# Kernel tuning notes

Hardware: AMD Instinct MI355X
Metric: run time of the kernel (lower is better)

The kernel has to match this reference:

```python
import jax, jax.numpy as jnp
import numpy as np

B, C, H, W = 4, 256, 64, 64
NHEAD = 8
KH = KW = 3          # partition = [3, 3] -> 9-token windows, stride 1, padding 1
EPS = 1e-5           # torch LayerNorm default


def setup_inputs() -> dict:
    key = jax.random.key(0)
    ks = jax.random.split(key, 3)
    s = 1.0 / np.sqrt(C)  # xavier-ish scale
    return {
        "src": jax.random.normal(ks[0], (B, C, H, W), jnp.float32),
        "ln_w": jnp.ones((C,), jnp.float32),
        "ln_b": jnp.zeros((C,), jnp.float32),
        "in_proj_w": jax.random.normal(ks[1], (3 * C, C), jnp.float32) * s,
        "in_proj_b": jnp.zeros((3 * C,), jnp.float32),
        "out_proj_w": jax.random.normal(ks[2], (C, C), jnp.float32) * s,
        "out_proj_b": jnp.zeros((C,), jnp.float32),
    }


def reference(src, ln_w, ln_b, in_proj_w, in_proj_b, out_proj_w, out_proj_b):
    b, c, h, w = src.shape
    L = h * w
    S = KH * KW  # 9 tokens per local window
    # --- Unfold: overlapping 3x3 windows, padding 1, stride 1 (torch.nn.Unfold order: c major, kernel pos minor)
    xp = jnp.pad(src, ((0, 0), (0, 0), (1, 1), (1, 1)))
    patches = jnp.stack(
        [xp[:, :, i : i + h, j : j + w] for i in range(KH) for j in range(KW)], axis=2
    )  # [b, c, 9, h, w]
    x = patches.reshape(b, c, S, L).transpose(2, 0, 3, 1).reshape(S, b * L, c)  # [S, bL, c]
    # --- Pre-norm (norm1); note: pos embed in the source is overwritten (q = k = src2), FFN is dead code
    mu = x.mean(-1, keepdims=True)
    var = ((x - mu) ** 2).mean(-1, keepdims=True)
    x2 = (x - mu) / jnp.sqrt(var + EPS) * ln_w + ln_b
    # --- MultiheadAttention (self-attn, eval mode -> no dropout)
    qkv = jnp.einsum("sbc,dc->sbd", x2, in_proj_w) + in_proj_b  # [S, bL, 3c]
    q, k, v = jnp.split(qkv, 3, axis=-1)
    dh = c // NHEAD
    scale = dh ** -0.5
    q = q.reshape(S, b * L, NHEAD, dh) * scale
    k = k.reshape(S, b * L, NHEAD, dh)
    v = v.reshape(S, b * L, NHEAD, dh)
    scores = jnp.einsum("sbhd,tbhd->bhst", q, k)        # [bL, H, 9, 9]
    attn = jax.nn.softmax(scores, axis=-1)
    o = jnp.einsum("bhst,tbhd->sbhd", attn, v).reshape(S, b * L, c)
    o = jnp.einsum("sbc,dc->sbd", o, out_proj_w) + out_proj_b
    y = x + o  # residual
    # --- Fold back (kernel 1x1, stride 1): each output pixel = its window's center token
    center = y[S // 2]  # [bL, c]
    return center.reshape(b, L, c).transpose(0, 2, 1).reshape(b, c, h, w)
```

## Files before the change

### kernel.cpp

```cpp
#include <hip/hip_runtime.h>
#include <math.h>


#define NPIX 16384
#define HW   4096
#define CDIM 256

typedef short  bf16x8 __attribute__((ext_vector_type(8)));
typedef float  f32x4  __attribute__((ext_vector_type(4)));
typedef unsigned short u16x8 __attribute__((ext_vector_type(8)));

__device__ inline float bf2f(unsigned short u) {
    unsigned v = ((unsigned)u) << 16;
    return __builtin_bit_cast(float, v);
}
__device__ inline unsigned short f2bf(float f) {
    unsigned u = __builtin_bit_cast(unsigned, f);
    u += 0x7FFFu + ((u >> 16) & 1u);
    return (unsigned short)(u >> 16);
}

__device__ inline void wave_fence_vm0() {
    asm volatile("s_waitcnt vmcnt(0)" ::: "memory");
    __builtin_amdgcn_sched_barrier(0);
}

__global__ __launch_bounds__(256) void k_prep(const float* __restrict__ Wqkv,
                                              const float* __restrict__ Wout,
                                              const float* __restrict__ bqkv,
                                              const float* __restrict__ lnb,
                                              unsigned short* __restrict__ Wqkvbf,
                                              unsigned short* __restrict__ Woutbf,
                                              float* __restrict__ pads) {
    int bid = blockIdx.x, t = threadIdx.x;
    if (bid < 768) {
        int i = bid * 256 + t;
        Wqkvbf[i] = f2bf(Wqkv[i]);
    } else if (bid < 1024) {
        int i = (bid - 768) * 256 + t;
        Woutbf[i] = f2bf(Wout[i]);
    } else {
        int tg = (bid - 1024) * 256 + t;
        int d = tg >> 4, part = tg & 15;
        int row = 256 + d;
        const float* wr = Wqkv + (size_t)row * CDIM + part * 16;
        float s = 0.f;
        #pragma unroll
        for (int c = 0; c < 16; ++c) s += lnb[part * 16 + c] * wr[c];
        s += __shfl_xor(s, 1);
        s += __shfl_xor(s, 2);
        s += __shfl_xor(s, 4);
        s += __shfl_xor(s, 8);
        if (part == 0) pads[d] = s + bqkv[row];
    }
}

__device__ inline void stage32(const unsigned short* __restrict__ g, int grow0,
                               int koff, unsigned short* dst, int lane) {
    int r16  = lane >> 2;
    int slot = lane & 3;
    #pragma unroll
    for (int it = 0; it < 4; ++it) {
        int row = it * 16 + r16;
        const unsigned short* src = g + (size_t)(grow0 + row) * 256 + koff
                                      + ((slot ^ ((row >> 1) & 3)) * 8);
        __builtin_amdgcn_global_load_lds(
            (const __attribute__((address_space(1))) void*)src,
            (__attribute__((address_space(3))) void*)(dst + it * 16 * 32),
            16, 0, 0);
    }
}

__global__ __launch_bounds__(256, 3) void k_ln_qkv(const float* __restrict__ src,
                                                   const float* __restrict__ lnw,
                                                   const float* __restrict__ lnb,
                                                   const unsigned short* __restrict__ Wbf,
                                                   const float* __restrict__ bias,
                                                   unsigned short* __restrict__ qkvbf) {
    __shared__ unsigned short As[32 * 256];
    __shared__ unsigned short Bs[4 * 4096];
    __shared__ float redS[8 * 33 * 2 + 64];

    int t = threadIdx.x;
    int bid = blockIdx.x;
    int sb = (bid & 7) * 64 + (bid >> 3);
    int n0 = sb * 32;
    int b = n0 >> 12, p0 = n0 & 4095;
    int lane = t & 63, wv = t >> 6;
    int lr = lane & 15, lg = lane >> 4;
    unsigned short* BsW = Bs + wv * 4096;

    stage32(Wbf, wv * 64, 0, BsW, lane);

    {
        float* red  = redS;
        float* red2 = redS + 264;
        float* muv  = redS + 528;
        float* rsv  = redS + 560;
        int pix = t & 31, q = t >> 5;
        const float* sp = src + ((size_t)b * CDIM) * HW + p0 + pix;
        float x[32];
        float sum = 0.f, sq = 0.f;
        #pragma unroll
        for (int i = 0; i < 32; ++i) {
            x[i] = sp[(size_t)(q * 32 + i) * HW];
            sum += x[i]; sq += x[i] * x[i];
        }
        red[q * 33 + pix] = sum; red2[q * 33 + pix] = sq;
        __syncthreads();
        if (t < 32) {
            float s = 0.f, s2 = 0.f;
            #pragma unroll
            for (int qq = 0; qq < 8; ++qq) { s += red[qq * 33 + t]; s2 += red2[qq * 33 + t]; }
            float mu = s * (1.f / 256.f);
            float var = fmaxf(s2 * (1.f / 256.f) - mu * mu, 0.f);
            muv[t] = mu; rsv[t] = rsqrtf(var + 1e-5f);
        }
        __syncthreads();
        float mu = muv[pix], rs = rsv[pix];
        #pragma unroll
        for (int c8 = 0; c8 < 4; ++c8) {
            u16x8 o8;
            #pragma unroll
            for (int j = 0; j < 8; ++j) {
                int c = q * 32 + c8 * 8 + j;
                float xn = (x[c8 * 8 + j] - mu) * rs * lnw[c] + lnb[c];
                o8[j] = f2bf(xn);
            }
            int chunk = q * 4 + c8;
            *(u16x8*)((char*)As + (pix * 512 + (((chunk & 7) ^ (pix & 7)) | (chunk & 24)) * 16)) = o8;
        }
    }
    __syncthreads();

    for (int pass = 0; pass < 3; ++pass) {
        int d0 = pass * 256;
        f32x4 acc[2][4] = {};
        #pragma unroll
        for (int kc = 0; kc < 8; ++kc) {
            int g = pass * 8 + kc;
            wave_fence_vm0();
            const unsigned short* B = BsW + (g & 1) * 2048;
            int chA = kc * 4 + lg;
            bf16x8 a[2], bb[4];
            #pragma unroll
            for (int i = 0; i < 2; ++i) {
                int r = i * 16 + lr;
                int sl = ((chA & 7) ^ (r & 7)) | (chA & 24);
                a[i] = *(bf16x8*)((char*)As + (r * 512 + sl * 16));
            }
            #pragma unroll
            for (int j = 0; j < 4; ++j) {
                int rb = j * 16 + lr;
                int sl = lg ^ ((rb >> 1) & 3);
                bb[j] = *(bf16x8*)(B + rb * 32 + sl * 8);
            }
            if (kc < 7)
                stage32(Wbf, d0 + wv * 64, (kc + 1) * 32,
                        BsW + ((g + 1) & 1) * 2048, lane);
            #pragma unroll
            for (int i = 0; i < 2; ++i)
                #pragma unroll
                for (int j = 0; j < 4; ++j)
                    acc[i][j] = __builtin_amdgcn_mfma_f32_16x16x32_bf16(
                        a[i], bb[j], acc[i][j], 0, 0, 0);
        }
        unsigned short* Ct = BsW;
        #pragma unroll
        for (int j = 0; j < 4; ++j) {
            float bj = bias[d0 + wv * 64 + j * 16 + lr];
            #pragma unroll
            for (int i = 0; i < 2; ++i)
                #pragma unroll
                for (int r2 = 0; r2 < 4; ++r2)
                    Ct[(i * 16 + lg * 4 + r2) * 72 + j * 16 + lr] =
                        f2bf(acc[i][j][r2] + bj);
        }
        #pragma unroll
        for (int it2 = 0; it2 < 4; ++it2) {
            int row = 8 * it2 + (lane >> 3);
            int chunk = lane & 7;
            bf16x8 v = *(bf16x8*)(Ct + row * 72 + chunk * 8);
            *(bf16x8*)(qkvbf + (size_t)(n0 + row) * 768 + d0 + wv * 64 + chunk * 8) = v;
        }
        if (pass < 2)
            stage32(Wbf, (pass + 1) * 256 + wv * 64, 0, BsW, lane);
    }
}

__global__ __launch_bounds__(256, 3) void k_attn_proj(const unsigned short* __restrict__ qkvbf,
                                                      const float* __restrict__ pads,
                                                      const unsigned short* __restrict__ Wbf,
                                                      const float* __restrict__ bias,
                                                      const float* __restrict__ src,
                                                      float* __restrict__ out) {
    __shared__ unsigned short Bt[32 * 264];
    __shared__ unsigned short Ws[4 * 4096];
    int t  = threadIdx.x;
    int bid = blockIdx.x;
    int sb  = (bid & 7) * 64 + (bid >> 3);
    int n0 = sb * 32;
    int b  = n0 >> 12;
    int p0 = n0 & 4095;
    int lane = t & 63, wv = t >> 6;
    int lr = lane & 15, lg = lane >> 4;
    unsigned short* WsW = Ws + wv * 4096;

    stage32(Wbf, wv * 64, 0, WsW, lane);

    {
        int pix = t >> 3, h = t & 7;
        int n = n0 + pix;
        int p = n & 4095, hh0 = p >> 6, ww0 = p & 63;
        const float scale = 0.1767766952966369f;

        float qv[32];
        const unsigned short* qp = qkvbf + (size_t)n * 768 + h * 32;
        #pragma unroll
        for (int c8 = 0; c8 < 4; ++c8) {
            bf16x8 v = *(const bf16x8*)(qp + c8 * 8);
            #pragma unroll
            for (int j = 0; j < 8; ++j) qv[c8 * 8 + j] = bf2f((unsigned short)v[j]) * scale;
        }
        float sc[9];
        #pragma unroll
        for (int t9 = 0; t9 < 9; ++t9) {
            int dy = t9 / 3 - 1, dx = t9 % 3 - 1;
            int hh = hh0 + dy, ww = ww0 + dx;
            bool ok = ((unsigned)hh < 64u) && ((unsigned)ww < 64u);
            float a = 0.f;
            if (ok) {
                const unsigned short* kp = qkvbf + (size_t)(n + dy * 64 + dx) * 768 + 256 + h * 32;
                #pragma unroll
                for (int c8 = 0; c8 < 4; ++c8) {
                    bf16x8 v = *(const bf16x8*)(kp + c8 * 8);
                    #pragma unroll
                    for (int j = 0; j < 8; ++j) a += qv[c8 * 8 + j] * bf2f((unsigned short)v[j]);
                }
            } else {
                const float* pk = pads + h * 32;
                #pragma unroll
                for (int j = 0; j < 32; ++j) a += qv[j] * pk[j];
            }
            sc[t9] = a;
        }
        float m = sc[0];
        #pragma unroll
        for (int t9 = 1; t9 < 9; ++t9) m = fmaxf(m, sc[t9]);
        float s = 0.f;
        #pragma unroll
        for (int t9 = 0; t9 < 9; ++t9) { sc[t9] = __expf(sc[t9] - m); s += sc[t9]; }
        float inv = 1.0f / s;

        float ov[32];
        #pragma unroll
        for (int j = 0; j < 32; ++j) ov[j] = 0.f;
        #pragma unroll
        for (int t9 = 0; t9 < 9; ++t9) {
            int dy = t9 / 3 - 1, dx = t9 % 3 - 1;
            int hh = hh0 + dy, ww = ww0 + dx;
            bool ok = ((unsigned)hh < 64u) && ((unsigned)ww < 64u);
            float w = sc[t9] * inv;
            if (ok) {
                const unsigned short* vp = qkvbf + (size_t)(n + dy * 64 + dx) * 768 + 512 + h * 32;
                #pragma unroll
                for (int c8 = 0; c8 < 4; ++c8) {
                    bf16x8 v = *(const bf16x8*)(vp + c8 * 8);
                    #pragma unroll
                    for (int j = 0; j < 8; ++j) ov[c8 * 8 + j] += w * bf2f((unsigned short)v[j]);
                }
            } else {
                const float* pv = pads + 256 + h * 32;
                #pragma unroll
                for (int j = 0; j < 32; ++j) ov[j] += w * pv[j];
            }
        }
        #pragma unroll
        for (int c8 = 0; c8 < 4; ++c8) {
            u16x8 o8;
            #pragma unroll
            for (int j = 0; j < 8; ++j) o8[j] = f2bf(ov[c8 * 8 + j]);
            *(u16x8*)(Bt + pix * 264 + h * 32 + c8 * 8) = o8;
        }
    }
    __syncthreads();

    f32x4 acc[4][2] = {};
    #pragma unroll
    for (int kc = 0; kc < 8; ++kc) {
        wave_fence_vm0();
        const unsigned short* A = WsW + (kc & 1) * 2048;
        bf16x8 a[4], bb[2];
        #pragma unroll
        for (int i = 0; i < 4; ++i) {
            int ri = i * 16 + lr;
            int sl = lg ^ ((ri >> 1) & 3);
            a[i] = *(bf16x8*)(A + ri * 32 + sl * 8);
        }
        #pragma unroll
        for (int j = 0; j < 2; ++j)
            bb[j] = *(bf16x8*)(Bt + (j * 16 + lr) * 264 + kc * 32 + lg * 8);
        if (kc < 7)
            stage32(Wbf, wv * 64, (kc + 1) * 32, WsW + ((kc + 1) & 1) * 2048, lane);
        #pragma unroll
        for (int i = 0; i < 4; ++i)
            #pragma unroll
            for (int j = 0; j < 2; ++j)
                acc[i][j] = __builtin_amdgcn_mfma_f32_16x16x32_bf16(
                    a[i], bb[j], acc[i][j], 0, 0, 0);
    }
    #pragma unroll
    for (int i = 0; i < 4; ++i) {
        #pragma unroll
        for (int r2 = 0; r2 < 4; ++r2) {
            int dg = wv * 64 + i * 16 + lg * 4 + r2;
            float bd = bias[dg];
            #pragma unroll
            for (int j = 0; j < 2; ++j) {
                int ng = p0 + j * 16 + lr;
                size_t idx = ((size_t)(b * CDIM + dg)) * HW + ng;
                out[idx] = acc[i][j][r2] + bd + src[idx];
            }
        }
    }
}

extern "C" void kernel_launch(void* const* d_in, const int* in_sizes, int n_in,
                              void* d_out, int out_size, void* d_ws, size_t ws_size,
                              hipStream_t stream) {
    const float* src  = (const float*)d_in[0];
    const float* lnw  = (const float*)d_in[1];
    const float* lnb  = (const float*)d_in[2];
    const float* Wqkv = (const float*)d_in[3];
    const float* bqkv = (const float*)d_in[4];
    const float* Wout = (const float*)d_in[5];
    const float* bout = (const float*)d_in[6];
    float* out = (float*)d_out;

    unsigned short* qkvbf  = (unsigned short*)d_ws;
    unsigned short* Wqkvbf = qkvbf + (size_t)NPIX * 768;
    unsigned short* Woutbf = Wqkvbf + 768 * 256;
    float* pads = (float*)(Woutbf + 256 * 256);

    k_prep<<<1056, 256, 0, stream>>>(Wqkv, Wout, bqkv, lnb, Wqkvbf, Woutbf, pads);
    k_ln_qkv<<<512, 256, 0, stream>>>(src, lnw, lnb, Wqkvbf, bqkv, qkvbf);
    k_attn_proj<<<512, 256, 0, stream>>>(qkvbf, pads, Woutbf, bout, src, out);
}
```

Before: 50.92 us.

## Issue next weight-tile loads before waiting and vectorize weight conversion

Both GEMM loops now issue the next weight-tile stage before consuming the current one and wait with vmcnt(4), so only the older loads must land. Previously every loaded tile was drained with vmcnt(0). MFMA blocks are bracketed with s_setprio, biases are hoisted into registers, and the epilogue staging buffer uses an XOR swizzle without padding, moved to the other half of the double buffer. The prep kernel converts weights with float4 loads in fewer blocks. This relies on the vmcnt count and the buffer reuse matching stage32's load count, which risks races if that count is wrong.

```diff
diff --git a/kernel.cpp b/kernel.cpp
--- a/kernel.cpp
+++ b/kernel.cpp
@@ -9,6 +9,7 @@
 typedef short  bf16x8 __attribute__((ext_vector_type(8)));
 typedef float  f32x4  __attribute__((ext_vector_type(4)));
 typedef unsigned short u16x8 __attribute__((ext_vector_type(8)));
+typedef unsigned short u16x4 __attribute__((ext_vector_type(4)));
 
 __device__ inline float bf2f(unsigned short u) {
     unsigned v = ((unsigned)u) << 16;
@@ -19,11 +20,7 @@
     u += 0x7FFFu + ((u >> 16) & 1u);
     return (unsigned short)(u >> 16);
 }
-
-__device__ inline void wave_fence_vm0() {
-    asm volatile("s_waitcnt vmcnt(0)" ::: "memory");
-    __builtin_amdgcn_sched_barrier(0);
-}
+__device__ inline void sb0() { __builtin_amdgcn_sched_barrier(0); }
 
 __global__ __launch_bounds__(256) void k_prep(const float* __restrict__ Wqkv,
                                               const float* __restrict__ Wout,
@@ -33,14 +30,18 @@
                                               unsigned short* __restrict__ Woutbf,
                                               float* __restrict__ pads) {
     int bid = blockIdx.x, t = threadIdx.x;
-    if (bid < 768) {
+    if (bid < 192) {
         int i = bid * 256 + t;
-        Wqkvbf[i] = f2bf(Wqkv[i]);
-    } else if (bid < 1024) {
-        int i = (bid - 768) * 256 + t;
-        Woutbf[i] = f2bf(Wout[i]);
+        float4 v = ((const float4*)Wqkv)[i];
+        u16x4 o = { f2bf(v.x), f2bf(v.y), f2bf(v.z), f2bf(v.w) };
+        *(u16x4*)(Wqkvbf + i * 4) = o;
+    } else if (bid < 256) {
+        int i = (bid - 192) * 256 + t;
+        float4 v = ((const float4*)Wout)[i];
+        u16x4 o = { f2bf(v.x), f2bf(v.y), f2bf(v.z), f2bf(v.w) };
+        *(u16x4*)(Woutbf + i * 4) = o;
     } else {
-        int tg = (bid - 1024) * 256 + t;
+        int tg = (bid - 256) * 256 + t;
         int d = tg >> 4, part = tg & 15;
         int row = 256 + d;
         const float* wr = Wqkv + (size_t)row * CDIM + part * 16;
@@ -92,6 +93,13 @@
 
     stage32(Wbf, wv * 64, 0, BsW, lane);
 
+    float bj[3][4];
+    #pragma unroll
+    for (int p = 0; p < 3; ++p)
+        #pragma unroll
+        for (int j = 0; j < 4; ++j)
+            bj[p][j] = bias[p * 256 + wv * 64 + j * 16 + lr];
+
     {
         float* red  = redS;
         float* red2 = redS + 264;
@@ -138,9 +146,19 @@
         f32x4 acc[2][4] = {};
         #pragma unroll
         for (int kc = 0; kc < 8; ++kc) {
-            int g = pass * 8 + kc;
-            wave_fence_vm0();
-            const unsigned short* B = BsW + (g & 1) * 2048;
+            sb0();
+            if (kc < 7) {
+                stage32(Wbf, d0 + wv * 64, (kc + 1) * 32,
+                        BsW + ((kc + 1) & 1) * 2048, lane);
+                asm volatile("s_waitcnt vmcnt(4)" ::: "memory");
+            } else if (pass < 2) {
+                stage32(Wbf, (pass + 1) * 256 + wv * 64, 0, BsW, lane);
+                asm volatile("s_waitcnt vmcnt(4)" ::: "memory");
+            } else {
+                asm volatile("s_waitcnt vmcnt(0)" ::: "memory");
+            }
+            sb0();
+            const unsigned short* B = BsW + (kc & 1) * 2048;
             int chA = kc * 4 + lg;
             bf16x8 a[2], bb[4];
             #pragma unroll
@@ -155,36 +173,38 @@
                 int sl = lg ^ ((rb >> 1) & 3);
                 bb[j] = *(bf16x8*)(B + rb * 32 + sl * 8);
             }
-            if (kc < 7)
-                stage32(Wbf, d0 + wv * 64, (kc + 1) * 32,
-                        BsW + ((g + 1) & 1) * 2048, lane);
+            __builtin_amdgcn_s_setprio(1);
             #pragma unroll
             for (int i = 0; i < 2; ++i)
                 #pragma unroll
                 for (int j = 0; j < 4; ++j)
                     acc[i][j] = __builtin_amdgcn_mfma_f32_16x16x32_bf16(
                         a[i], bb[j], acc[i][j], 0, 0, 0);
-        }
-        unsigned short* Ct = BsW;
+            __builtin_amdgcn_s_setprio(0);
+        }
+        sb0();
+        unsigned short* Ct = BsW + 2048;
         #pragma unroll
         for (int j = 0; j < 4; ++j) {
-            float bj = bias[d0 + wv * 64 + j * 16 + lr];
             #pragma unroll
             for (int i = 0; i < 2; ++i)
                 #pragma unroll
-                for (int r2 = 0; r2 < 4; ++r2)
-                    Ct[(i * 16 + lg * 4 + r2) * 72 + j * 16 + lr] =
-                        f2bf(acc[i][j][r2] + bj);
+                for (int r2 = 0; r2 < 4; ++r2) {
+                    int row = i * 16 + lg * 4 + r2;
+                    int col = j * 16 + lr;
+                    int ch  = col >> 3;
+                    int sl  = ch ^ (row & 7);
+                    Ct[row * 64 + sl * 8 + (col & 7)] = f2bf(acc[i][j][r2] + bj[pass][j]);
+                }
         }
         #pragma unroll
         for (int it2 = 0; it2 < 4; ++it2) {
             int row = 8 * it2 + (lane >> 3);
             int chunk = lane & 7;
-            bf16x8 v = *(bf16x8*)(Ct + row * 72 + chunk * 8);
+            int sl = chunk ^ (row & 7);
+            bf16x8 v = *(bf16x8*)(Ct + row * 64 + sl * 8);
             *(bf16x8*)(qkvbf + (size_t)(n0 + row) * 768 + d0 + wv * 64 + chunk * 8) = v;
         }
-        if (pass < 2)
-            stage32(Wbf, (pass + 1) * 256 + wv * 64, 0, BsW, lane);
     }
 }
 
@@ -208,6 +228,13 @@
 
     stage32(Wbf, wv * 64, 0, WsW, lane);
 
+    float bd[4][4];
+    #pragma unroll
+    for (int i = 0; i < 4; ++i)
+        #pragma unroll
+        for (int r2 = 0; r2 < 4; ++r2)
+            bd[i][r2] = bias[wv * 64 + i * 16 + lg * 4 + r2];
+
     {
         int pix = t >> 3, h = t & 7;
         int n = n0 + pix;
@@ -288,7 +315,14 @@
     f32x4 acc[4][2] = {};
     #pragma unroll
     for (int kc = 0; kc < 8; ++kc) {
-        wave_fence_vm0();
+        sb0();
+        if (kc < 7) {
+            stage32(Wbf, wv * 64, (kc + 1) * 32, WsW + ((kc + 1) & 1) * 2048, lane);
+            asm volatile("s_waitcnt vmcnt(4)" ::: "memory");
+        } else {
+            asm volatile("s_waitcnt vmcnt(0)" ::: "memory");
+        }
+        sb0();
         const unsigned short* A = WsW + (kc & 1) * 2048;
         bf16x8 a[4], bb[2];
         #pragma unroll
@@ -300,26 +334,25 @@
         #pragma unroll
         for (int j = 0; j < 2; ++j)
             bb[j] = *(bf16x8*)(Bt + (j * 16 + lr) * 264 + kc * 32 + lg * 8);
-        if (kc < 7)
-            stage32(Wbf, wv * 64, (kc + 1) * 32, WsW + ((kc + 1) & 1) * 2048, lane);
+        __builtin_amdgcn_s_setprio(1);
         #pragma unroll
         for (int i = 0; i < 4; ++i)
             #pragma unroll
             for (int j = 0; j < 2; ++j)
                 acc[i][j] = __builtin_amdgcn_mfma_f32_16x16x32_bf16(
                     a[i], bb[j], acc[i][j], 0, 0, 0);
+        __builtin_amdgcn_s_setprio(0);
     }
     #pragma unroll
     for (int i = 0; i < 4; ++i) {
         #pragma unroll
         for (int r2 = 0; r2 < 4; ++r2) {
             int dg = wv * 64 + i * 16 + lg * 4 + r2;
-            float bd = bias[dg];
             #pragma unroll
             for (int j = 0; j < 2; ++j) {
                 int ng = p0 + j * 16 + lr;
                 size_t idx = ((size_t)(b * CDIM + dg)) * HW + ng;
-                out[idx] = acc[i][j][r2] + bd + src[idx];
+                out[idx] = acc[i][j][r2] + bd[i][r2] + src[idx];
             }
         }
     }
@@ -342,7 +375,7 @@
     unsigned short* Woutbf = Wqkvbf + 768 * 256;
     float* pads = (float*)(Woutbf + 256 * 256);
 
-    k_prep<<<1056, 256, 0, stream>>>(Wqkv, Wout, bqkv, lnb, Wqkvbf, Woutbf, pads);
+    k_prep<<<288, 256, 0, stream>>>(Wqkv, Wout, bqkv, lnb, Wqkvbf, Woutbf, pads);
     k_ln_qkv<<<512, 256, 0, stream>>>(src, lnw, lnb, Wqkvbf, bqkv, qkvbf);
     k_attn_proj<<<512, 256, 0, stream>>>(qkvbf, pads, Woutbf, bout, src, out);
 }
```

After: 51.25 us. Within noise of the previous version (+0.6%).
